# Kernel tuning notes

Measured on AMD Instinct MI355X. Metric: run time of the kernel, lower is better.

Reference implementation:

```python
import jax, jax.numpy as jnp
import numpy as np

# Qwen3-0.6B-like config; 4 equal-length requests flattened into [R*S, H]
L, R, S, H = 2, 4, 1024, 1024
NH, NKV, DH = 16, 8, 128
FF = 3072
EPS = 1e-6
THETA = 1e6
SCALE = 0.02  # weight init scale to keep activations sane


def setup_inputs() -> dict:
    key = jax.random.key(0)
    ks = jax.random.split(key, 8)
    return {
        "hidden_states": jax.random.normal(ks[0], (R * S, H), jnp.float32),
        "Wq": jax.random.normal(ks[1], (L, H, NH * DH), jnp.float32) * SCALE,
        "Wk": jax.random.normal(ks[2], (L, H, NKV * DH), jnp.float32) * SCALE,
        "Wv": jax.random.normal(ks[3], (L, H, NKV * DH), jnp.float32) * SCALE,
        "Wo": jax.random.normal(ks[4], (L, NH * DH, H), jnp.float32) * SCALE,
        "q_norm_w": jnp.ones((L, DH), jnp.float32),
        "k_norm_w": jnp.ones((L, DH), jnp.float32),
        "ln1_w": jnp.ones((L, H), jnp.float32),
        "ln2_w": jnp.ones((L, H), jnp.float32),
        "Wg": jax.random.normal(ks[5], (L, H, FF), jnp.float32) * SCALE,
        "Wu": jax.random.normal(ks[6], (L, H, FF), jnp.float32) * SCALE,
        "Wd": jax.random.normal(ks[7], (L, FF, H), jnp.float32) * SCALE,
        "final_norm_w": jnp.ones((H,), jnp.float32),
    }


def _rms(x, w):
    return x * jax.lax.rsqrt(jnp.mean(x * x, axis=-1, keepdims=True) + EPS) * w


def _rope_tables():
    inv_freq = 1.0 / (THETA ** (jnp.arange(0, DH, 2, dtype=jnp.float32) / DH))
    pos = jnp.arange(S, dtype=jnp.float32)  # per-request positions 0..S-1 (prefill)
    freqs = pos[:, None] * inv_freq[None, :]        # [S, DH/2]
    emb = jnp.concatenate([freqs, freqs], axis=-1)  # [S, DH]
    return jnp.cos(emb), jnp.sin(emb)


def _rotate_half(x):
    x1, x2 = jnp.split(x, 2, axis=-1)
    return jnp.concatenate([-x2, x1], axis=-1)


def _apply_rope(x, cos, sin):
    # x: [R, heads, S, DH]; cos/sin: [S, DH]
    c = cos[None, None]
    s = sin[None, None]
    return x * c + _rotate_half(x) * s


def reference(hidden_states, Wq, Wk, Wv, Wo, q_norm_w, k_norm_w, ln1_w, ln2_w,
              Wg, Wu, Wd, final_norm_w):
    cos, sin = _rope_tables()
    causal = jnp.tril(jnp.ones((S, S), dtype=bool))  # per-request causal mask
    neg = jnp.finfo(hidden_states.dtype).min
    scaling = 1.0 / jnp.sqrt(jnp.asarray(DH, hidden_states.dtype))

    x = hidden_states
    for l in range(L):
        # --- attention block ---
        residual = x
        h = _rms(x, ln1_w[l])                       # [R*S, H]
        q = (h @ Wq[l]).reshape(R, S, NH, DH)
        k = (h @ Wk[l]).reshape(R, S, NKV, DH)
        v = (h @ Wv[l]).reshape(R, S, NKV, DH)
        q = _rms(q, q_norm_w[l]).transpose(0, 2, 1, 3)   # [R, NH, S, DH]
        k = _rms(k, k_norm_w[l]).transpose(0, 2, 1, 3)   # [R, NKV, S, DH]
        v = v.transpose(0, 2, 1, 3)                      # [R, NKV, S, DH]
        q = _apply_rope(q, cos, sin)
        k = _apply_rope(k, cos, sin)
        # GQA: repeat KV heads
        rep = NH // NKV
        k = jnp.repeat(k, rep, axis=1)
        v = jnp.repeat(v, rep, axis=1)
        scores = jnp.einsum('rhqd,rhkd->rhqk', q, k) * scaling
        scores = jnp.where(causal[None, None], scores, neg)
        attn = jax.nn.softmax(scores, axis=-1)
        o = jnp.einsum('rhqk,rhkd->rhqd', attn, v)       # [R, NH, S, DH]
        o = o.transpose(0, 2, 1, 3).reshape(R * S, NH * DH)
        x = residual + o @ Wo[l]
        # --- MLP block ---
        residual = x
        h = _rms(x, ln2_w[l])
        x = residual + (jax.nn.silu(h @ Wg[l]) * (h @ Wu[l])) @ Wd[l]
    return _rms(x, final_norm_w)
```

## Files before the change

kernel.cpp:

```cpp
#include <hip/hip_runtime.h>
#include <hip/hip_bf16.h>

typedef __bf16 bf16;
typedef __bf16 bf16x8 __attribute__((ext_vector_type(8)));
typedef float f32x4 __attribute__((ext_vector_type(4)));

#define DEVINL __device__ __forceinline__

constexpr int L_ = 2, R_ = 4, S_ = 1024, H_ = 1024;
constexpr int NH_ = 16, NKV_ = 8, DH_ = 128;
constexpr int FF_ = 3072;
constexpr int T_ = R_ * S_;

DEVINL void gload16(const bf16* g, bf16* l) {
    __builtin_amdgcn_global_load_lds(
        (const __attribute__((address_space(1))) void*)g,
        (__attribute__((address_space(3))) void*)l, 16, 0, 0);
}

__global__ void rope_tables_kernel(float* __restrict__ cosb, float* __restrict__ sinb) {
    int s = blockIdx.x;
    int i = threadIdx.x;
    float inv = __expf(-(float)i * (1.0f / 64.0f) * 13.815510557964274f);
    float f = (float)s * inv;
    cosb[s * 64 + i] = cosf(f);
    sinb[s * 64 + i] = sinf(f);
}

template <bool OUT_BF16>
__global__ __launch_bounds__(256) void rmsnorm_kernel(const float* __restrict__ x,
                                                      const float* __restrict__ w,
                                                      void* __restrict__ out) {
    int row = blockIdx.x;
    const float* xr = x + (size_t)row * H_;
    int t = threadIdx.x;
    float v[4];
    float ss = 0.f;
#pragma unroll
    for (int j = 0; j < 4; ++j) {
        v[j] = xr[t + 256 * j];
        ss += v[j] * v[j];
    }
#pragma unroll
    for (int off = 32; off; off >>= 1) ss += __shfl_xor(ss, off);
    __shared__ float part[4];
    if ((t & 63) == 0) part[t >> 6] = ss;
    __syncthreads();
    ss = part[0] + part[1] + part[2] + part[3];
    float r = rsqrtf(ss * (1.0f / (float)H_) + 1e-6f);
#pragma unroll
    for (int j = 0; j < 4; ++j) {
        int c = t + 256 * j;
        float o = v[j] * r * w[c];
        if constexpr (OUT_BF16)
            ((bf16*)out)[(size_t)row * H_ + c] = (bf16)o;
        else
            ((float*)out)[(size_t)row * H_ + c] = o;
    }
}

__global__ __launch_bounds__(256) void transpose_cast_kernel(const float* __restrict__ in,
                                                             bf16* __restrict__ out,
                                                             int Rk, int Cn, int mode) {
    __shared__ float tile[32][33];
    int c0 = blockIdx.x * 32, r0 = blockIdx.y * 32;
    int t = threadIdx.x;
    int tc = t & 31, tr = t >> 5;
#pragma unroll
    for (int i = 0; i < 4; ++i) {
        int r = tr + i * 8;
        tile[r][tc] = in[(size_t)(r0 + r) * Cn + c0 + tc];
    }
    __syncthreads();
#pragma unroll
    for (int i = 0; i < 4; ++i) {
        int c = c0 + tr + i * 8;
        int n = (mode == 0) ? c : (((c >> 4) << 5) + ((mode == 2) ? 16 : 0) + (c & 15));
        out[(size_t)n * Rk + r0 + tc] = (bf16)tile[tc][tr + i * 8];
    }
}

__global__ __launch_bounds__(256) void vt_kernel(const bf16* __restrict__ qkv,
                                                 bf16* __restrict__ vt) {
    __shared__ bf16 tile[32][34];
    int s0 = blockIdx.x * 32, c0 = blockIdx.y * 32, r = blockIdx.z;
    int t = threadIdx.x, tc = t & 31, tr = t >> 5;
#pragma unroll
    for (int i = 0; i < 4; ++i) {
        int s = tr + i * 8;
        tile[s][tc] = qkv[(size_t)(r * 1024 + s0 + s) * 4096 + 3072 + c0 + tc];
    }
    __syncthreads();
#pragma unroll
    for (int i = 0; i < 4; ++i) {
        int c = tr + i * 8;
        vt[((size_t)(r * 1024 + c0 + c)) * 1024 + s0 + tc] = tile[tc][c];
    }
}

template <int EPI>
__global__ __launch_bounds__(512, 2) void gemmQ_kernel(const bf16* __restrict__ A,
                                                       const bf16* __restrict__ Bt,
                                                       void* __restrict__ out,
                                                       int M, int N, int K) {
    __shared__ bf16 lds[49152];
    const int NT = K >> 5;
    int nbm = M >> 8, nbn = N >> 8;
    int slice = nbn >> 3;
    int id = blockIdx.x;
    int xcd = id & 7, wi = id >> 3;
    int bm = (wi % nbm) << 8, bn = (xcd * slice + wi / nbm) << 8;
    int t = threadIdx.x, lane = t & 63, w = t >> 6;
    int wm = w >> 2, wn = w & 3;
    int hi = lane >> 4, f = lane & 15;

    int srow = t >> 2;
    int ssc = (t & 3) ^ ((srow >> 1) & 3);
    const bf16* a0 = A + (size_t)(bm + srow) * K + (ssc << 3);
    const bf16* a1 = A + (size_t)(bm + 128 + srow) * K + (ssc << 3);
    const bf16* b0 = Bt + (size_t)(bn + srow) * K + (ssc << 3);
    const bf16* b1 = Bt + (size_t)(bn + 128 + srow) * K + (ssc << 3);

    f32x4 acc[8][4] = {};

    auto stage = [&](int tt, int sb) {
        gload16(a0 + tt * 32, lds + sb * 8192 + w * 512);
        gload16(a1 + tt * 32, lds + sb * 8192 + 4096 + w * 512);
        gload16(b0 + tt * 32, lds + 24576 + sb * 8192 + w * 512);
        gload16(b1 + tt * 32, lds + 24576 + sb * 8192 + 4096 + w * 512);
    };

    stage(0, 0);
    stage(1, 1);
    asm volatile("s_waitcnt vmcnt(4)" ::: "memory");
    __builtin_amdgcn_s_barrier();

    int cb = 0;
    for (int tau = 0; tau < NT; ++tau) {
        const bf16* aB = lds + cb * 8192;
        const bf16* bB = lds + 24576 + cb * 8192;
        if (tau + 2 < NT) stage(tau + 2, (cb == 0) ? 2 : cb - 1);
        bf16x8 af[8], bfv[4];
#pragma unroll
        for (int mf = 0; mf < 8; ++mf) {
            int row = wm * 128 + mf * 16 + f;
            af[mf] = *(const bf16x8*)(aB + row * 32 + ((hi ^ ((row >> 1) & 3)) << 3));
        }
#pragma unroll
        for (int nf = 0; nf < 4; ++nf) {
            int row = wn * 64 + nf * 16 + f;
            bfv[nf] = *(const bf16x8*)(bB + row * 32 + ((hi ^ ((row >> 1) & 3)) << 3));
        }
        __builtin_amdgcn_s_setprio(1);
#pragma unroll
        for (int mf = 0; mf < 8; ++mf)
#pragma unroll
            for (int nf = 0; nf < 4; ++nf)
                acc[mf][nf] = __builtin_amdgcn_mfma_f32_16x16x32_bf16(af[mf], bfv[nf],
                                                                      acc[mf][nf], 0, 0, 0);
        __builtin_amdgcn_s_setprio(0);
        if (tau < NT - 2)
            asm volatile("s_waitcnt vmcnt(4)" ::: "memory");
        else
            asm volatile("s_waitcnt vmcnt(0)" ::: "memory");
        __builtin_amdgcn_s_barrier();
        cb = (cb == 2) ? 0 : cb + 1;
    }

    int rb = bm + wm * 128 + hi * 4;
    int cb2 = bn + wn * 64 + f;
#pragma unroll
    for (int mf = 0; mf < 8; ++mf)
#pragma unroll
        for (int nf = 0; nf < 4; ++nf)
#pragma unroll
            for (int g = 0; g < 4; ++g)
                ((bf16*)out)[(size_t)(rb + mf * 16 + g) * N + cb2 + nf * 16] =
                    (bf16)acc[mf][nf][g];
}

template <int EPI>
__global__ __launch_bounds__(512, 4) void gemmP_kernel(const bf16* __restrict__ A,
                                                       const bf16* __restrict__ Bt,
                                                       void* __restrict__ out,
                                                       int M, int N, int K) {
    __shared__ bf16 lds[36864];
    const int NT = K >> 5;
    int nbm = M >> 7, nbn = N >> 8;
    int slice = nbn >> 3;
    int id = blockIdx.x;
    int xcd = id & 7, wi = id >> 3;
    int bm = (wi % nbm) << 7, bn = (xcd * slice + wi / nbm) << 8;
    int t = threadIdx.x, lane = t & 63, w = t >> 6;
    int wm = w >> 2, wn = w & 3;
    int hi = lane >> 4, f = lane & 15;

    int srow = t >> 2;
    int ssc = (t & 3) ^ ((srow >> 1) & 3);
    const bf16* aSrc = A + (size_t)(bm + srow) * K + (ssc << 3);
    const bf16* b0Src = Bt + (size_t)(bn + srow) * K + (ssc << 3);
    const bf16* b1Src = Bt + (size_t)(bn + 128 + srow) * K + (ssc << 3);

    f32x4 acc[4][4] = {};

    auto stage = [&](int tt, int sb) {
        gload16(aSrc + tt * 32, lds + sb * 4096 + w * 512);
        gload16(b0Src + tt * 32, lds + 12288 + sb * 8192 + w * 512);
        gload16(b1Src + tt * 32, lds + 12288 + sb * 8192 + 4096 + w * 512);
    };

    stage(0, 0);
    stage(1, 1);
    asm volatile("s_waitcnt vmcnt(3)" ::: "memory");
    __builtin_amdgcn_s_barrier();

    int cb = 0;
    for (int tau = 0; tau < NT; ++tau) {
        const bf16* aB = lds + cb * 4096;
        const bf16* bB = lds + 12288 + cb * 8192;
        if (tau + 2 < NT) stage(tau + 2, (cb == 0) ? 2 : cb - 1);
        bf16x8 af[4], bfv[4];
#pragma unroll
        for (int mf = 0; mf < 4; ++mf) {
            int row = wm * 64 + mf * 16 + f;
            af[mf] = *(const bf16x8*)(aB + row * 32 + ((hi ^ ((row >> 1) & 3)) << 3));
        }
#pragma unroll
        for (int nf = 0; nf < 4; ++nf) {
            int row = wn * 64 + nf * 16 + f;
            bfv[nf] = *(const bf16x8*)(bB + row * 32 + ((hi ^ ((row >> 1) & 3)) << 3));
        }
        __builtin_amdgcn_s_setprio(1);
#pragma unroll
        for (int mf = 0; mf < 4; ++mf)
#pragma unroll
            for (int nf = 0; nf < 4; ++nf)
                acc[mf][nf] = __builtin_amdgcn_mfma_f32_16x16x32_bf16(af[mf], bfv[nf],
                                                                      acc[mf][nf], 0, 0, 0);
        __builtin_amdgcn_s_setprio(0);
        if (tau < NT - 2)
            asm volatile("s_waitcnt vmcnt(3)" ::: "memory");
        else
            asm volatile("s_waitcnt vmcnt(0)" ::: "memory");
        __builtin_amdgcn_s_barrier();
        cb = (cb == 2) ? 0 : cb + 1;
    }

    int rb = bm + wm * 64 + hi * 4;
#pragma unroll
    for (int mf = 0; mf < 4; ++mf) {
        if constexpr (EPI == 5) {
#pragma unroll
            for (int p = 0; p < 2; ++p) {
                int col = ((bn + wn * 64) >> 1) + p * 16 + f;
#pragma unroll
                for (int g = 0; g < 4; ++g) {
                    float gv = acc[mf][2 * p][g], uv = acc[mf][2 * p + 1][g];
                    float sv = gv / (1.0f + __expf(-gv));
                    ((bf16*)out)[(size_t)(rb + mf * 16 + g) * (N / 2) + col] = (bf16)(sv * uv);
                }
            }
        } else {
            int cb2 = bn + wn * 64 + f;
#pragma unroll
            for (int nf = 0; nf < 4; ++nf)
#pragma unroll
                for (int g = 0; g < 4; ++g)
                    ((bf16*)out)[(size_t)(rb + mf * 16 + g) * N + cb2 + nf * 16] =
                        (bf16)acc[mf][nf][g];
        }
    }
}

template <int EPI>
__global__ __launch_bounds__(256, 2) void gemmD_kernel(const bf16* __restrict__ A,
                                                       const bf16* __restrict__ Bt,
                                                       void* __restrict__ out,
                                                       const float* __restrict__ res,
                                                       int M, int N, int K) {
    __shared__ bf16 lds[36864];
    const int NT = K >> 6;
    int nbm = M >> 6;
    int id = blockIdx.x;
    int xcd = id & 7, wi = id >> 3;
    int bm = (wi % nbm) << 6, bn = xcd << 7;
    int t = threadIdx.x, lane = t & 63, w = t >> 6;
    int wm = w >> 1, wn = w & 1;
    int hi = lane >> 4, f = lane & 15;

    int ar0 = t >> 3, ac0 = t & 7;
    const bf16* aS0 = A + (size_t)(bm + ar0) * K + (((ac0 ^ (ar0 & 7)) & 7) << 3);
    const bf16* aS1 = A + (size_t)(bm + 32 + ar0) * K + (((ac0 ^ ((ar0 + 32) & 7)) & 7) << 3);
    const bf16* bS[4];
#pragma unroll
    for (int j = 0; j < 4; ++j) {
        int row = j * 32 + ar0;
        bS[j] = Bt + (size_t)(bn + row) * K + (((ac0 ^ (row & 7)) & 7) << 3);
    }

    f32x4 acc[2][4] = {};

    auto stage = [&](int tt, int sb) {
        gload16(aS0 + tt * 64, lds + sb * 4096 + w * 512);
        gload16(aS1 + tt * 64, lds + sb * 4096 + 2048 + w * 512);
#pragma unroll
        for (int j = 0; j < 4; ++j)
            gload16(bS[j] + tt * 64, lds + 12288 + sb * 8192 + j * 2048 + w * 512);
    };

    stage(0, 0);
    stage(1, 1);
    asm volatile("s_waitcnt vmcnt(6)" ::: "memory");
    __builtin_amdgcn_s_barrier();

    int cb = 0;
    for (int tau = 0; tau < NT; ++tau) {
        const bf16* aB = lds + cb * 4096;
        const bf16* bB = lds + 12288 + cb * 8192;
        if (tau + 2 < NT) stage(tau + 2, (cb == 0) ? 2 : cb - 1);
        bf16x8 af[2][2], bfv[2][4];
#pragma unroll
        for (int kh = 0; kh < 2; ++kh) {
            int q = kh * 4 + hi;
#pragma unroll
            for (int mf = 0; mf < 2; ++mf) {
                int row = wm * 32 + mf * 16 + f;
                af[kh][mf] = *(const bf16x8*)(aB + row * 64 + ((q ^ (row & 7)) << 3));
            }
#pragma unroll
            for (int nf = 0; nf < 4; ++nf) {
                int row = wn * 64 + nf * 16 + f;
                bfv[kh][nf] = *(const bf16x8*)(bB + row * 64 + ((q ^ (row & 7)) << 3));
            }
        }
        __builtin_amdgcn_s_setprio(1);
#pragma unroll
        for (int kh = 0; kh < 2; ++kh)
#pragma unroll
            for (int mf = 0; mf < 2; ++mf)
#pragma unroll
                for (int nf = 0; nf < 4; ++nf)
                    acc[mf][nf] = __builtin_amdgcn_mfma_f32_16x16x32_bf16(
                        af[kh][mf], bfv[kh][nf], acc[mf][nf], 0, 0, 0);
        __builtin_amdgcn_s_setprio(0);
        if (tau < NT - 2)
            asm volatile("s_waitcnt vmcnt(6)" ::: "memory");
        else
            asm volatile("s_waitcnt vmcnt(0)" ::: "memory");
        __builtin_amdgcn_s_barrier();
        cb = (cb == 2) ? 0 : cb + 1;
    }

    int rb = bm + wm * 32 + hi * 4;
    int cb2 = bn + wn * 64 + f;
#pragma unroll
    for (int mf = 0; mf < 2; ++mf)
#pragma unroll
        for (int nf = 0; nf < 4; ++nf)
#pragma unroll
            for (int g = 0; g < 4; ++g) {
                size_t idx = (size_t)(rb + mf * 16 + g) * N + cb2 + nf * 16;
                ((float*)out)[idx] = acc[mf][nf][g] + res[idx];
            }
}

DEVINL void head_norm_rope(const bf16* __restrict__ src, const float* __restrict__ w,
                           const float* __restrict__ cosb, const float* __restrict__ sinb,
                           int s, int ln, bf16* __restrict__ dst) {
    float x0 = (float)src[ln], x1 = (float)src[ln + 32];
    float x2 = (float)src[ln + 64], x3 = (float)src[ln + 96];
    float ss = x0 * x0 + x1 * x1 + x2 * x2 + x3 * x3;
#pragma unroll
    for (int off = 16; off; off >>= 1) ss += __shfl_xor(ss, off);
    float rr = rsqrtf(ss * (1.0f / 128.0f) + 1e-6f);
    float n0 = x0 * rr * w[ln], n1 = x1 * rr * w[ln + 32];
    float n2 = x2 * rr * w[ln + 64], n3 = x3 * rr * w[ln + 96];
    float c0 = cosb[s * 64 + ln], c1 = cosb[s * 64 + ln + 32];
    float s0 = sinb[s * 64 + ln], s1 = sinb[s * 64 + ln + 32];
    dst[ln] = (bf16)(n0 * c0 - n2 * s0);
    dst[ln + 32] = (bf16)(n1 * c1 - n3 * s1);
    dst[ln + 64] = (bf16)(n2 * c0 + n0 * s0);
    dst[ln + 96] = (bf16)(n3 * c1 + n1 * s1);
}

__global__ __launch_bounds__(256) void qkv_post_kernel(const bf16* __restrict__ qkv,
                                                       const float* __restrict__ qw,
                                                       const float* __restrict__ kw,
                                                       const float* __restrict__ cosb,
                                                       const float* __restrict__ sinb,
                                                       bf16* __restrict__ qo,
                                                       bf16* __restrict__ ko) {
    int tok = blockIdx.x;
    int r = tok >> 10, s = tok & 1023;
    int t = threadIdx.x;
    int g = t >> 5;
    int ln = t & 31;
    const bf16* row = qkv + (size_t)tok * 4096;
#pragma unroll
    for (int hh = 0; hh < 2; ++hh) {
        int h = g + hh * 8;
        head_norm_rope(row + h * 128, qw, cosb, sinb, s, ln,
                       qo + ((size_t)(r * NH_ + h) * S_ + s) * 128);
    }
    head_norm_rope(row + 2048 + g * 128, kw, cosb, sinb, s, ln,
                   ko + ((size_t)(r * NKV_ + g) * S_ + s) * 128);
}

__global__ __launch_bounds__(256, 2) void flash_kernel(const bf16* __restrict__ q,
                                                       const bf16* __restrict__ k,
                                                       const bf16* __restrict__ vt,
                                                       bf16* __restrict__ out) {
    __shared__ bf16 Kl[64 * 128];
    __shared__ bf16 Vl[128 * 64];
    __shared__ bf16 Pl[4][32][72];
    int bid = blockIdx.x;
    int grp = bid & 63, slot = bid >> 6;
    int strip = (slot < 4) ? (7 - slot) : (slot - 4);
    int h = 2 * (grp & 7) + ((grp >> 3) & 1);
    int r = grp >> 4;
    int kvh = h >> 1;

    int t = threadIdx.x, lane = t & 63, w = t >> 6;
    int arow = lane & 15, hi = lane >> 4;
    int a7 = arow & 7;
    int grow = hi * 4;
    int qbase = strip * 128 + w * 32;

    const bf16* qp = q + ((size_t)(r * NH_ + h) * S_ + qbase) * 128;
    bf16x8 qf[2][4];
#pragma unroll
    for (int m = 0; m < 2; ++m)
#pragma unroll
        for (int kc = 0; kc < 4; ++kc)
            qf[m][kc] = *(const bf16x8*)(qp + (size_t)(m * 16 + arow) * 128 + kc * 32 + hi * 8);

    const bf16* kp = k + (size_t)(r * NKV_ + kvh) * S_ * 128;
    const bf16* vp = vt + (size_t)(r * NKV_ + kvh) * 128 * S_;

    int krow0 = t >> 4, kc16 = t & 15;
    int vrow0 = t >> 3, vc16 = t & 7;

    f32x4 ao[2][8] = {};
    float mrow[2][4], lrow[2][4];
#pragma unroll
    for (int m = 0; m < 2; ++m)
#pragma unroll
        for (int g = 0; g < 4; ++g) { mrow[m][g] = -1e30f; lrow[m][g] = 0.f; }
    const float scale = 0.08838834764831845f;

    int nt = 2 * (strip + 1);
    bf16x8 krs[4], vrs[4];
#pragma unroll
    for (int i = 0; i < 4; ++i)
        krs[i] = *(const bf16x8*)(kp + (size_t)(krow0 + 16 * i) * 128 + kc16 * 8);
#pragma unroll
    for (int i = 0; i < 4; ++i)
        vrs[i] = *(const bf16x8*)(vp + (size_t)(vrow0 + 32 * i) * S_ + vc16 * 8);

    for (int it = 0; it < nt; ++it) {
        int kv0 = it * 64;
        __syncthreads();
#pragma unroll
        for (int i = 0; i < 4; ++i) {
            int row = krow0 + 16 * i;
            *(bf16x8*)(&Kl[row * 128 + ((kc16 ^ (row & 7)) * 8)]) = krs[i];
        }
#pragma unroll
        for (int i = 0; i < 4; ++i) {
            int row = vrow0 + 32 * i;
            *(bf16x8*)(&Vl[row * 64 + ((vc16 ^ (row & 7)) * 8)]) = vrs[i];
        }
        __syncthreads();
        if (it + 1 < nt) {
            int kvn = kv0 + 64;
#pragma unroll
            for (int i = 0; i < 4; ++i)
                krs[i] = *(const bf16x8*)(kp + (size_t)(kvn + krow0 + 16 * i) * 128 + kc16 * 8);
#pragma unroll
            for (int i = 0; i < 4; ++i)
                vrs[i] = *(const bf16x8*)(vp + (size_t)(vrow0 + 32 * i) * S_ + kvn + vc16 * 8);
        }
        f32x4 sc[2][4];
#pragma unroll
        for (int m = 0; m < 2; ++m)
#pragma unroll
            for (int n = 0; n < 4; ++n) sc[m][n] = (f32x4){0.f, 0.f, 0.f, 0.f};
#pragma unroll
        for (int n = 0; n < 4; ++n) {
            int krw = n * 16 + arow;
#pragma unroll
            for (int kc = 0; kc < 4; ++kc) {
                bf16x8 kf = *(const bf16x8*)(&Kl[krw * 128 + (((kc * 4 + hi) ^ a7) * 8)]);
                sc[0][n] = __builtin_amdgcn_mfma_f32_16x16x32_bf16(qf[0][kc], kf, sc[0][n], 0, 0, 0);
                sc[1][n] = __builtin_amdgcn_mfma_f32_16x16x32_bf16(qf[1][kc], kf, sc[1][n], 0, 0, 0);
            }
        }
#pragma unroll
        for (int m = 0; m < 2; ++m) {
            float pm[4][4];
            bool msk = (kv0 + 64 > qbase + m * 16);
#pragma unroll
            for (int n = 0; n < 4; ++n)
#pragma unroll
                for (int g = 0; g < 4; ++g) {
                    float sval = sc[m][n][g] * scale;
                    if (msk && (kv0 + n * 16 + arow > qbase + m * 16 + grow + g)) sval = -1e30f;
                    pm[n][g] = sval;
                }
            float mx[4], sf[4], rs[4];
#pragma unroll
            for (int g = 0; g < 4; ++g)
                mx[g] = fmaxf(fmaxf(pm[0][g], pm[1][g]), fmaxf(pm[2][g], pm[3][g]));
#pragma unroll
            for (int off = 8; off; off >>= 1)
#pragma unroll
                for (int g = 0; g < 4; ++g) mx[g] = fmaxf(mx[g], __shfl_xor(mx[g], off));
#pragma unroll
            for (int g = 0; g < 4; ++g) {
                float mnew = fmaxf(mrow[m][g], mx[g]);
                sf[g] = __expf(mrow[m][g] - mnew);
                mrow[m][g] = mnew;
            }
#pragma unroll
            for (int n = 0; n < 4; ++n)
#pragma unroll
                for (int g = 0; g < 4; ++g) pm[n][g] = __expf(pm[n][g] - mrow[m][g]);
#pragma unroll
            for (int g = 0; g < 4; ++g) rs[g] = pm[0][g] + pm[1][g] + pm[2][g] + pm[3][g];
#pragma unroll
            for (int off = 8; off; off >>= 1)
#pragma unroll
                for (int g = 0; g < 4; ++g) rs[g] += __shfl_xor(rs[g], off);
#pragma unroll
            for (int g = 0; g < 4; ++g) lrow[m][g] = lrow[m][g] * sf[g] + rs[g];
#pragma unroll
            for (int c = 0; c < 8; ++c)
#pragma unroll
                for (int g = 0; g < 4; ++g) ao[m][c][g] *= sf[g];
#pragma unroll
            for (int n = 0; n < 4; ++n)
#pragma unroll
                for (int g = 0; g < 4; ++g)
                    Pl[w][m * 16 + grow + g][n * 16 + arow] = (bf16)pm[n][g];
        }
        bf16x8 pf[2][2];
#pragma unroll
        for (int m = 0; m < 2; ++m)
#pragma unroll
            for (int ks = 0; ks < 2; ++ks)
                pf[m][ks] = *(const bf16x8*)(&Pl[w][m * 16 + arow][ks * 32 + hi * 8]);
#pragma unroll
        for (int c = 0; c < 8; ++c) {
            int vrw = c * 16 + arow;
#pragma unroll
            for (int ks = 0; ks < 2; ++ks) {
                bf16x8 vf = *(const bf16x8*)(&Vl[vrw * 64 + (((ks * 4 + hi) ^ a7) * 8)]);
                ao[0][c] = __builtin_amdgcn_mfma_f32_16x16x32_bf16(pf[0][ks], vf, ao[0][c], 0, 0, 0);
                ao[1][c] = __builtin_amdgcn_mfma_f32_16x16x32_bf16(pf[1][ks], vf, ao[1][c], 0, 0, 0);
            }
        }
    }
#pragma unroll
    for (int m = 0; m < 2; ++m)
#pragma unroll
        for (int c = 0; c < 8; ++c)
#pragma unroll
            for (int g = 0; g < 4; ++g) {
                int rq = qbase + m * 16 + grow + g;
                out[(size_t)(r * S_ + rq) * 2048 + h * 128 + c * 16 + arow] =
                    (bf16)(ao[m][c][g] / lrow[m][g]);
            }
}

extern "C" void kernel_launch(void* const* d_in, const int* in_sizes, int n_in,
                              void* d_out, int out_size, void* d_ws, size_t ws_size,
                              hipStream_t stream) {
    const float* hidden = (const float*)d_in[0];
    const float* Wq = (const float*)d_in[1];
    const float* Wk = (const float*)d_in[2];
    const float* Wv = (const float*)d_in[3];
    const float* Wo = (const float*)d_in[4];
    const float* qnw = (const float*)d_in[5];
    const float* knw = (const float*)d_in[6];
    const float* ln1 = (const float*)d_in[7];
    const float* ln2 = (const float*)d_in[8];
    const float* Wg = (const float*)d_in[9];
    const float* Wu = (const float*)d_in[10];
    const float* Wd = (const float*)d_in[11];
    const float* fnw = (const float*)d_in[12];
    float* out = (float*)d_out;

    char* ws = (char*)d_ws;
    size_t off = 0;
    auto alloc = [&](size_t bytes) -> char* {
        char* p = ws + off;
        off += (bytes + 255) & ~(size_t)255;
        return p;
    };
    float* cosb = (float*)alloc((size_t)S_ * 64 * 4);
    float* sinb = (float*)alloc((size_t)S_ * 64 * 4);
    float* x_ws = (float*)alloc((size_t)T_ * H_ * 4);
    bf16* hbuf = (bf16*)alloc((size_t)T_ * H_ * 2);
    bf16* qkv = (bf16*)alloc((size_t)T_ * 4096 * 2);
    bf16* act = qkv;
    bf16* qb = (bf16*)alloc((size_t)R_ * NH_ * S_ * 128 * 2);
    bf16* kb = (bf16*)alloc((size_t)R_ * NKV_ * S_ * 128 * 2);
    bf16* vtb = (bf16*)alloc((size_t)R_ * NKV_ * 128 * S_ * 2);
    bf16* attn = (bf16*)alloc((size_t)T_ * 2048 * 2);
    bf16* wqkv_t = (bf16*)alloc((size_t)4096 * 1024 * 2);
    bf16* wo_t = (bf16*)alloc((size_t)1024 * 2048 * 2);
    bf16* wgu_t = (bf16*)alloc((size_t)6144 * 1024 * 2);
    bf16* wd_t = (bf16*)alloc((size_t)1024 * 3072 * 2);

    rope_tables_kernel<<<S_, 64, 0, stream>>>(cosb, sinb);

    const float* xin = hidden;
    for (int l = 0; l < L_; ++l) {
        transpose_cast_kernel<<<dim3(2048 / 32, 1024 / 32), 256, 0, stream>>>(
            Wq + (size_t)l * H_ * 2048, wqkv_t, 1024, 2048, 0);
        transpose_cast_kernel<<<dim3(1024 / 32, 1024 / 32), 256, 0, stream>>>(
            Wk + (size_t)l * H_ * 1024, wqkv_t + (size_t)2048 * 1024, 1024, 1024, 0);
        transpose_cast_kernel<<<dim3(1024 / 32, 1024 / 32), 256, 0, stream>>>(
            Wv + (size_t)l * H_ * 1024, wqkv_t + (size_t)3072 * 1024, 1024, 1024, 0);
        transpose_cast_kernel<<<dim3(1024 / 32, 2048 / 32), 256, 0, stream>>>(
            Wo + (size_t)l * 2048 * 1024, wo_t, 2048, 1024, 0);
        transpose_cast_kernel<<<dim3(3072 / 32, 1024 / 32), 256, 0, stream>>>(
            Wg + (size_t)l * H_ * 3072, wgu_t, 1024, 3072, 1);
        transpose_cast_kernel<<<dim3(3072 / 32, 1024 / 32), 256, 0, stream>>>(
            Wu + (size_t)l * H_ * 3072, wgu_t, 1024, 3072, 2);
        transpose_cast_kernel<<<dim3(1024 / 32, 3072 / 32), 256, 0, stream>>>(
            Wd + (size_t)l * 3072 * 1024, wd_t, 3072, 1024, 0);

        rmsnorm_kernel<true><<<T_, 256, 0, stream>>>(xin, ln1 + (size_t)l * H_, hbuf);
        gemmQ_kernel<1><<<256, 512, 0, stream>>>(hbuf, wqkv_t, qkv, 4096, 4096, 1024);
        qkv_post_kernel<<<T_, 256, 0, stream>>>(qkv, qnw + (size_t)l * 128, knw + (size_t)l * 128,
                                                cosb, sinb, qb, kb);
        vt_kernel<<<dim3(32, 32, 4), 256, 0, stream>>>(qkv, vtb);
        flash_kernel<<<512, 256, 0, stream>>>(qb, kb, vtb, attn);
        gemmD_kernel<4><<<512, 256, 0, stream>>>(attn, wo_t, x_ws, xin, 4096, 1024, 2048);
        rmsnorm_kernel<true><<<T_, 256, 0, stream>>>(x_ws, ln2 + (size_t)l * H_, hbuf);
        gemmP_kernel<5><<<768, 512, 0, stream>>>(hbuf, wgu_t, act, 4096, 6144, 1024);
        gemmD_kernel<4><<<512, 256, 0, stream>>>(act, wd_t, x_ws, x_ws, 4096, 1024, 3072);
        xin = x_ws;
    }
    rmsnorm_kernel<false><<<T_, 256, 0, stream>>>(x_ws, fnw, out);
}
```

Before: 541.5 us.

## Merge weight transposes into one launch and split 256x256 GEMM into two phases

All seven per-layer weight transpose/cast launches are replaced by a single kernel that picks its source matrix from the block index, cutting launch overhead. The 256x256 gemmQ main loop is split into two half-M phases, with A and B prefetch loads interleaved between them and extra barriers added, so loads overlap MFMA work and fewer A fragments are live at once. The gate/up GEMM now uses this 256x256 kernel with the SiLU epilogue instead of the 128x256 gemmP kernel, halving its grid. The added barriers and the larger tile could cost occupancy or add stalls.

```diff
diff --git a/kernel.cpp b/kernel.cpp
--- a/kernel.cpp
+++ b/kernel.cpp
@@ -6,6 +6,7 @@
 typedef float f32x4 __attribute__((ext_vector_type(4)));
 
 #define DEVINL __device__ __forceinline__
+#define SBAR() asm volatile("s_barrier" ::: "memory")
 
 constexpr int L_ = 2, R_ = 4, S_ = 1024, H_ = 1024;
 constexpr int NH_ = 16, NKV_ = 8, DH_ = 128;
@@ -59,11 +60,25 @@
     }
 }
 
-__global__ __launch_bounds__(256) void transpose_cast_kernel(const float* __restrict__ in,
-                                                             bf16* __restrict__ out,
-                                                             int Rk, int Cn, int mode) {
+__global__ __launch_bounds__(256) void transpose_all_kernel(
+    const float* __restrict__ Wq, const float* __restrict__ Wk, const float* __restrict__ Wv,
+    const float* __restrict__ Wo, const float* __restrict__ Wg, const float* __restrict__ Wu,
+    const float* __restrict__ Wd, bf16* __restrict__ wqkv_t, bf16* __restrict__ wo_t,
+    bf16* __restrict__ wgu_t, bf16* __restrict__ wd_t) {
     __shared__ float tile[32][33];
-    int c0 = blockIdx.x * 32, r0 = blockIdx.y * 32;
+    int bid = blockIdx.x;
+    const float* in;
+    bf16* out;
+    int Rk, Cn, mode, tid;
+    if (bid < 2048) { in = Wq; out = wqkv_t; Rk = 1024; Cn = 2048; mode = 0; tid = bid; }
+    else if (bid < 3072) { in = Wk; out = wqkv_t + (size_t)2048 * 1024; Rk = 1024; Cn = 1024; mode = 0; tid = bid - 2048; }
+    else if (bid < 4096) { in = Wv; out = wqkv_t + (size_t)3072 * 1024; Rk = 1024; Cn = 1024; mode = 0; tid = bid - 3072; }
+    else if (bid < 6144) { in = Wo; out = wo_t; Rk = 2048; Cn = 1024; mode = 0; tid = bid - 4096; }
+    else if (bid < 9216) { in = Wg; out = wgu_t; Rk = 1024; Cn = 3072; mode = 1; tid = bid - 6144; }
+    else if (bid < 12288) { in = Wu; out = wgu_t; Rk = 1024; Cn = 3072; mode = 2; tid = bid - 9216; }
+    else { in = Wd; out = wd_t; Rk = 3072; Cn = 1024; mode = 0; tid = bid - 12288; }
+    int nbx = Cn >> 5;
+    int c0 = (tid % nbx) * 32, r0 = (tid / nbx) * 32;
     int t = threadIdx.x;
     int tc = t & 31, tr = t >> 5;
 #pragma unroll
@@ -123,26 +138,28 @@
 
     f32x4 acc[8][4] = {};
 
-    auto stage = [&](int tt, int sb) {
-        gload16(a0 + tt * 32, lds + sb * 8192 + w * 512);
-        gload16(a1 + tt * 32, lds + sb * 8192 + 4096 + w * 512);
-        gload16(b0 + tt * 32, lds + 24576 + sb * 8192 + w * 512);
-        gload16(b1 + tt * 32, lds + 24576 + sb * 8192 + 4096 + w * 512);
-    };
-
-    stage(0, 0);
-    stage(1, 1);
+    gload16(a0, lds + 0 * 8192 + w * 512);
+    gload16(a1, lds + 0 * 8192 + 4096 + w * 512);
+    gload16(b0, lds + 24576 + 0 * 8192 + w * 512);
+    gload16(b1, lds + 24576 + 0 * 8192 + 4096 + w * 512);
+    gload16(a0 + 32, lds + 1 * 8192 + w * 512);
+    gload16(a1 + 32, lds + 1 * 8192 + 4096 + w * 512);
+    gload16(b0 + 32, lds + 24576 + 1 * 8192 + w * 512);
+    gload16(b1 + 32, lds + 24576 + 1 * 8192 + 4096 + w * 512);
     asm volatile("s_waitcnt vmcnt(4)" ::: "memory");
-    __builtin_amdgcn_s_barrier();
+    SBAR();
 
     int cb = 0;
     for (int tau = 0; tau < NT; ++tau) {
         const bf16* aB = lds + cb * 8192;
         const bf16* bB = lds + 24576 + cb * 8192;
-        if (tau + 2 < NT) stage(tau + 2, (cb == 0) ? 2 : cb - 1);
-        bf16x8 af[8], bfv[4];
-#pragma unroll
-        for (int mf = 0; mf < 8; ++mf) {
+        int sb = (cb == 0) ? 2 : cb - 1;
+        bool doStage = (tau + 2 < NT);
+        int tt = tau + 2;
+
+        bf16x8 af[4], bfv[4];
+#pragma unroll
+        for (int mf = 0; mf < 4; ++mf) {
             int row = wm * 128 + mf * 16 + f;
             af[mf] = *(const bf16x8*)(aB + row * 32 + ((hi ^ ((row >> 1) & 3)) << 3));
         }
@@ -151,104 +168,51 @@
             int row = wn * 64 + nf * 16 + f;
             bfv[nf] = *(const bf16x8*)(bB + row * 32 + ((hi ^ ((row >> 1) & 3)) << 3));
         }
+        if (doStage) {
+            gload16(a0 + tt * 32, lds + sb * 8192 + w * 512);
+            gload16(a1 + tt * 32, lds + sb * 8192 + 4096 + w * 512);
+        }
+        SBAR();
         __builtin_amdgcn_s_setprio(1);
 #pragma unroll
-        for (int mf = 0; mf < 8; ++mf)
+        for (int mf = 0; mf < 4; ++mf)
 #pragma unroll
             for (int nf = 0; nf < 4; ++nf)
                 acc[mf][nf] = __builtin_amdgcn_mfma_f32_16x16x32_bf16(af[mf], bfv[nf],
                                                                       acc[mf][nf], 0, 0, 0);
+        __builtin_amdgcn_s_setprio(0);
+        SBAR();
+
+        bf16x8 af2[4];
+#pragma unroll
+        for (int mf = 0; mf < 4; ++mf) {
+            int row = wm * 128 + (mf + 4) * 16 + f;
+            af2[mf] = *(const bf16x8*)(aB + row * 32 + ((hi ^ ((row >> 1) & 3)) << 3));
+        }
+        if (doStage) {
+            gload16(b0 + tt * 32, lds + 24576 + sb * 8192 + w * 512);
+            gload16(b1 + tt * 32, lds + 24576 + sb * 8192 + 4096 + w * 512);
+        }
+        SBAR();
+        __builtin_amdgcn_s_setprio(1);
+#pragma unroll
+        for (int mf = 0; mf < 4; ++mf)
+#pragma unroll
+            for (int nf = 0; nf < 4; ++nf)
+                acc[mf + 4][nf] = __builtin_amdgcn_mfma_f32_16x16x32_bf16(af2[mf], bfv[nf],
+                                                                          acc[mf + 4][nf], 0, 0, 0);
         __builtin_amdgcn_s_setprio(0);
         if (tau < NT - 2)
             asm volatile("s_waitcnt vmcnt(4)" ::: "memory");
         else
             asm volatile("s_waitcnt vmcnt(0)" ::: "memory");
-        __builtin_amdgcn_s_barrier();
+        SBAR();
         cb = (cb == 2) ? 0 : cb + 1;
     }
 
     int rb = bm + wm * 128 + hi * 4;
-    int cb2 = bn + wn * 64 + f;
-#pragma unroll
-    for (int mf = 0; mf < 8; ++mf)
-#pragma unroll
-        for (int nf = 0; nf < 4; ++nf)
-#pragma unroll
-            for (int g = 0; g < 4; ++g)
-                ((bf16*)out)[(size_t)(rb + mf * 16 + g) * N + cb2 + nf * 16] =
-                    (bf16)acc[mf][nf][g];
-}
-
-template <int EPI>
-__global__ __launch_bounds__(512, 4) void gemmP_kernel(const bf16* __restrict__ A,
-                                                       const bf16* __restrict__ Bt,
-                                                       void* __restrict__ out,
-                                                       int M, int N, int K) {
-    __shared__ bf16 lds[36864];
-    const int NT = K >> 5;
-    int nbm = M >> 7, nbn = N >> 8;
-    int slice = nbn >> 3;
-    int id = blockIdx.x;
-    int xcd = id & 7, wi = id >> 3;
-    int bm = (wi % nbm) << 7, bn = (xcd * slice + wi / nbm) << 8;
-    int t = threadIdx.x, lane = t & 63, w = t >> 6;
-    int wm = w >> 2, wn = w & 3;
-    int hi = lane >> 4, f = lane & 15;
-
-    int srow = t >> 2;
-    int ssc = (t & 3) ^ ((srow >> 1) & 3);
-    const bf16* aSrc = A + (size_t)(bm + srow) * K + (ssc << 3);
-    const bf16* b0Src = Bt + (size_t)(bn + srow) * K + (ssc << 3);
-    const bf16* b1Src = Bt + (size_t)(bn + 128 + srow) * K + (ssc << 3);
-
-    f32x4 acc[4][4] = {};
-
-    auto stage = [&](int tt, int sb) {
-        gload16(aSrc + tt * 32, lds + sb * 4096 + w * 512);
-        gload16(b0Src + tt * 32, lds + 12288 + sb * 8192 + w * 512);
-        gload16(b1Src + tt * 32, lds + 12288 + sb * 8192 + 4096 + w * 512);
-    };
-
-    stage(0, 0);
-    stage(1, 1);
-    asm volatile("s_waitcnt vmcnt(3)" ::: "memory");
-    __builtin_amdgcn_s_barrier();
-
-    int cb = 0;
-    for (int tau = 0; tau < NT; ++tau) {
-        const bf16* aB = lds + cb * 4096;
-        const bf16* bB = lds + 12288 + cb * 8192;
-        if (tau + 2 < NT) stage(tau + 2, (cb == 0) ? 2 : cb - 1);
-        bf16x8 af[4], bfv[4];
-#pragma unroll
-        for (int mf = 0; mf < 4; ++mf) {
-            int row = wm * 64 + mf * 16 + f;
-            af[mf] = *(const bf16x8*)(aB + row * 32 + ((hi ^ ((row >> 1) & 3)) << 3));
-        }
-#pragma unroll
-        for (int nf = 0; nf < 4; ++nf) {
-            int row = wn * 64 + nf * 16 + f;
-            bfv[nf] = *(const bf16x8*)(bB + row * 32 + ((hi ^ ((row >> 1) & 3)) << 3));
-        }
-        __builtin_amdgcn_s_setprio(1);
-#pragma unroll
-        for (int mf = 0; mf < 4; ++mf)
-#pragma unroll
-            for (int nf = 0; nf < 4; ++nf)
-                acc[mf][nf] = __builtin_amdgcn_mfma_f32_16x16x32_bf16(af[mf], bfv[nf],
-                                                                      acc[mf][nf], 0, 0, 0);
-        __builtin_amdgcn_s_setprio(0);
-        if (tau < NT - 2)
-            asm volatile("s_waitcnt vmcnt(3)" ::: "memory");
-        else
-            asm volatile("s_waitcnt vmcnt(0)" ::: "memory");
-        __builtin_amdgcn_s_barrier();
-        cb = (cb == 2) ? 0 : cb + 1;
-    }
-
-    int rb = bm + wm * 64 + hi * 4;
-#pragma unroll
-    for (int mf = 0; mf < 4; ++mf) {
+#pragma unroll
+    for (int mf = 0; mf < 8; ++mf) {
         if constexpr (EPI == 5) {
 #pragma unroll
             for (int p = 0; p < 2; ++p) {
@@ -616,20 +580,10 @@
 
     const float* xin = hidden;
     for (int l = 0; l < L_; ++l) {
-        transpose_cast_kernel<<<dim3(2048 / 32, 1024 / 32), 256, 0, stream>>>(
-            Wq + (size_t)l * H_ * 2048, wqkv_t, 1024, 2048, 0);
-        transpose_cast_kernel<<<dim3(1024 / 32, 1024 / 32), 256, 0, stream>>>(
-            Wk + (size_t)l * H_ * 1024, wqkv_t + (size_t)2048 * 1024, 1024, 1024, 0);
-        transpose_cast_kernel<<<dim3(1024 / 32, 1024 / 32), 256, 0, stream>>>(
-            Wv + (size_t)l * H_ * 1024, wqkv_t + (size_t)3072 * 1024, 1024, 1024, 0);
-        transpose_cast_kernel<<<dim3(1024 / 32, 2048 / 32), 256, 0, stream>>>(
-            Wo + (size_t)l * 2048 * 1024, wo_t, 2048, 1024, 0);
-        transpose_cast_kernel<<<dim3(3072 / 32, 1024 / 32), 256, 0, stream>>>(
-            Wg + (size_t)l * H_ * 3072, wgu_t, 1024, 3072, 1);
-        transpose_cast_kernel<<<dim3(3072 / 32, 1024 / 32), 256, 0, stream>>>(
-            Wu + (size_t)l * H_ * 3072, wgu_t, 1024, 3072, 2);
-        transpose_cast_kernel<<<dim3(1024 / 32, 3072 / 32), 256, 0, stream>>>(
-            Wd + (size_t)l * 3072 * 1024, wd_t, 3072, 1024, 0);
+        transpose_all_kernel<<<15360, 256, 0, stream>>>(
+            Wq + (size_t)l * H_ * 2048, Wk + (size_t)l * H_ * 1024, Wv + (size_t)l * H_ * 1024,
+            Wo + (size_t)l * 2048 * 1024, Wg + (size_t)l * H_ * 3072, Wu + (size_t)l * H_ * 3072,
+            Wd + (size_t)l * 3072 * 1024, wqkv_t, wo_t, wgu_t, wd_t);
 
         rmsnorm_kernel<true><<<T_, 256, 0, stream>>>(xin, ln1 + (size_t)l * H_, hbuf);
         gemmQ_kernel<1><<<256, 512, 0, stream>>>(hbuf, wqkv_t, qkv, 4096, 4096, 1024);
@@ -639,7 +593,7 @@
         flash_kernel<<<512, 256, 0, stream>>>(qb, kb, vtb, attn);
         gemmD_kernel<4><<<512, 256, 0, stream>>>(attn, wo_t, x_ws, xin, 4096, 1024, 2048);
         rmsnorm_kernel<true><<<T_, 256, 0, stream>>>(x_ws, ln2 + (size_t)l * H_, hbuf);
-        gemmP_kernel<5><<<768, 512, 0, stream>>>(hbuf, wgu_t, act, 4096, 6144, 1024);
+        gemmQ_kernel<5><<<384, 512, 0, stream>>>(hbuf, wgu_t, act, 4096, 6144, 1024);
         gemmD_kernel<4><<<512, 256, 0, stream>>>(act, wd_t, x_ws, x_ws, 4096, 1024, 3072);
         xin = x_ws;
     }
```

Result: no change. 552.0 us (+1.9%).
